# Optimization experiments

Hardware: AMD Instinct MI355X
Metric: run time of the kernel (lower is better)

## Reference

```python
import jax, jax.numpy as jnp
import numpy as np

B, C, H, W = 32, 64, 64, 64
K = 512  # n_embeddings
D = 64   # embedding_dim


def setup_inputs() -> dict:
    key = jax.random.key(0)
    k1, k2 = jax.random.split(key)
    inputs = jax.random.normal(k1, (B, C, H, W), dtype=jnp.float32)
    embedding = jax.random.normal(k2, (K, D), dtype=jnp.float32)
    weight = jnp.ones((K,), dtype=jnp.float32)
    return {"inputs": inputs, "embedding": embedding, "weight": weight}


def reference(inputs, embedding, weight):
    # NCHW -> NHWC, flatten to [N, D]
    x = jnp.transpose(inputs, (0, 2, 3, 1))  # [B,H,W,D]
    input_shape = x.shape
    flat = x.reshape(-1, D)                  # [N,D], N = B*H*W
    n = flat.shape[0]

    usage = jnp.sum(weight >= 0.01)

    # squared Euclidean distances (argmin-equivalent to torch.cdist)
    d2 = (jnp.sum(flat * flat, axis=1, keepdims=True)
          - 2.0 * (flat @ embedding.T)
          + jnp.sum(embedding * embedding, axis=1))  # [N,K]
    indices = jnp.argmin(d2, axis=1)                 # [N]

    # one-hot assignment stats (scatter -> bincount form)
    counts = jnp.zeros((K,), dtype=flat.dtype).at[indices].add(1.0)
    avg_probs = counts / n
    perplexity = jnp.exp(-jnp.sum(avg_probs * jnp.log(avg_probs + 1e-10)))

    # straight-through quantization
    q = embedding[indices].reshape(input_shape)      # [B,H,W,D]
    quantized = jax.lax.stop_gradient(q) + x - jax.lax.stop_gradient(x)

    commitment_loss = jnp.mean((jax.lax.stop_gradient(quantized) - x) ** 2)

    quantized_nchw = jnp.transpose(quantized, (0, 3, 1, 2))
    return quantized_nchw, commitment_loss, perplexity, usage, indices
```

## Files before the change

### kernel.cpp

```cpp
#include <hip/hip_runtime.h>


typedef __attribute__((ext_vector_type(8))) _Float16 f16x8;
typedef __attribute__((ext_vector_type(4))) float f32x4;
typedef unsigned int uint;
typedef unsigned short ushort;

namespace {
constexpr int kC = 64, kH = 64, kW = 64;
constexpr int kK = 512, kD = 64;
constexpr int kHW = kH * kW;
constexpr int kCHW = kC * kHW;
constexpr int kN = 32 * kHW;
constexpr int kQElems = 32 * kC * kHW;
constexpr uint kGapFP = 21u;
}

__device__ __forceinline__ ushort hb(_Float16 h) { return __builtin_bit_cast(ushort, h); }
__device__ __forceinline__ uint umin(uint a, uint b) { return a < b ? a : b; }
__device__ __forceinline__ uint umax(uint a, uint b) { return a > b ? a : b; }

__device__ __forceinline__ void gld16(const void* g, void* l) {
  __builtin_amdgcn_global_load_lds(
      (const __attribute__((address_space(1))) uint*)g,
      (__attribute__((address_space(3))) uint*)l, 16, 0, 0);
}

__global__ __launch_bounds__(64) void vq_prep(const float* __restrict__ emb,
                                              ushort* __restrict__ embPh,
                                              ushort* __restrict__ embPl,
                                              float* __restrict__ embT,
                                              float* __restrict__ enorm,
                                              uint* __restrict__ counts,
                                              uint* __restrict__ flag_count) {
  const int k = blockIdx.x * 64 + threadIdx.x;
  const float4* __restrict__ ep4 = (const float4*)(emb + k * kD);
  float ev[kD];
  uint uh[32], ul[32];
  float s = 0.f;
#pragma unroll
  for (int j = 0; j < kD / 4; ++j) {
    const float4 v = ep4[j];
    ev[4 * j] = v.x; ev[4 * j + 1] = v.y; ev[4 * j + 2] = v.z; ev[4 * j + 3] = v.w;
    s = fmaf(v.x, v.x, s); s = fmaf(v.y, v.y, s);
    s = fmaf(v.z, v.z, s); s = fmaf(v.w, v.w, s);
#pragma unroll
    for (int t = 0; t < 2; ++t) {
      const float e0 = ev[4 * j + 2 * t] * 2048.f;
      const float e1 = ev[4 * j + 2 * t + 1] * 2048.f;
      const _Float16 h0 = (_Float16)e0, h1 = (_Float16)e1;
      const _Float16 l0 = (_Float16)(e0 - (float)h0);
      const _Float16 l1 = (_Float16)(e1 - (float)h1);
      uh[2 * j + t] = (uint)hb(h0) | ((uint)hb(h1) << 16);
      ul[2 * j + t] = (uint)hb(l0) | ((uint)hb(l1) << 16);
    }
  }
  uint4* __restrict__ ph4 = (uint4*)embPh;
  uint4* __restrict__ pl4 = (uint4*)embPl;
#pragma unroll
  for (int cc = 0; cc < 8; ++cc) {
    const int dst = k * 8 + (cc ^ (k & 7));
    ph4[dst] = uint4{uh[4 * cc], uh[4 * cc + 1], uh[4 * cc + 2], uh[4 * cc + 3]};
    pl4[dst] = uint4{ul[4 * cc], ul[4 * cc + 1], ul[4 * cc + 2], ul[4 * cc + 3]};
  }
#pragma unroll
  for (int c = 0; c < kD; ++c) embT[c * kK + k] = ev[c];
  enorm[k] = s;
  counts[k] = 0u;
  if (k == 0) *flag_count = 0u;
}

__global__ __launch_bounds__(512, 4) void vq_assign(
    const float* __restrict__ in, const ushort* __restrict__ embPh,
    const ushort* __restrict__ embPl, const float* __restrict__ embT,
    const float* __restrict__ enorm, float* __restrict__ idx_out,
    float* __restrict__ outq, uint* __restrict__ counts,
    float* __restrict__ partial, uint* __restrict__ flag_count,
    uint* __restrict__ flags, uint flag_cap) {
  __shared__ __align__(16) ushort xbh[128 * 64];
  __shared__ __align__(16) ushort xbl[128 * 64];
  __shared__ __align__(16) ushort ebh[2][4096];
  __shared__ __align__(16) ushort ebl[2][4096];
  __shared__ uint mm1[4][128], mm2[4][128];
  __shared__ float xnp[4][128];
  __shared__ uint hist[512];
  __shared__ uint fidx[128];

  const int tid = threadIdx.x;
  const int lane = tid & 63;
  const int wv = __builtin_amdgcn_readfirstlane(tid >> 6);
  const int ph = wv >> 2;
  const int cs = wv & 3;
  const int c = lane & 15;
  const int g = lane >> 4;

  const int blk = blockIdx.x;
  const int bb = blk >> 5;
  const int hw0 = (blk & 31) << 7;
  const float* __restrict__ xp = in + (size_t)bb * kCHW + hw0 + ph * 64;

  hist[tid] = 0u;

  auto stageE = [&](int buf, int st) {
    const char* gh = (const char*)embPh + st * 8192 + wv * 1024 + lane * 16;
    const char* gl = (const char*)embPl + st * 8192 + wv * 1024 + lane * 16;
    gld16(gh, (char*)&ebh[buf][0] + wv * 1024);
    gld16(gl, (char*)&ebl[buf][0] + wv * 1024);
  };
  stageE(0, 0);

  float en_pre[8];
#pragma unroll
  for (int st = 0; st < 8; ++st)
    en_pre[st] = (enorm[st * 64 + cs * 16 + c] + 256.f) * 2048.f;

  {
    const int p = lane;
    uint uh[8], ul[8];
    float xn = 0.f;
#pragma unroll
    for (int j = 0; j < 8; ++j) {
      const float f0 = xp[(size_t)(cs * 16 + 2 * j) * kHW + p];
      const float f1 = xp[(size_t)(cs * 16 + 2 * j + 1) * kHW + p];
      xn = fmaf(f0, f0, xn);
      xn = fmaf(f1, f1, xn);
      const float m0 = -2.f * f0, m1f = -2.f * f1;
      const _Float16 h0 = (_Float16)m0, h1 = (_Float16)m1f;
      const _Float16 l0 = (_Float16)(m0 - (float)h0);
      const _Float16 l1 = (_Float16)(m1f - (float)h1);
      uh[j] = (uint)hb(h0) | ((uint)hb(h1) << 16);
      ul[j] = (uint)hb(l0) | ((uint)hb(l1) << 16);
    }
    const int row = ph * 64 + p;
    const int swz = (row & 7) << 4;
    const int o0 = (row * 128 + cs * 32) ^ swz;
    const int o1 = (row * 128 + cs * 32 + 16) ^ swz;
    *(uint4*)((char*)xbh + o0) = uint4{uh[0], uh[1], uh[2], uh[3]};
    *(uint4*)((char*)xbh + o1) = uint4{uh[4], uh[5], uh[6], uh[7]};
    *(uint4*)((char*)xbl + o0) = uint4{ul[0], ul[1], ul[2], ul[3]};
    *(uint4*)((char*)xbl + o1) = uint4{ul[4], ul[5], ul[6], ul[7]};
    xnp[cs][row] = xn;
  }
  __syncthreads();

  f16x8 ah[4][2];
  int aoff[4][2];
#pragma unroll
  for (int rt = 0; rt < 4; ++rt)
#pragma unroll
    for (int s = 0; s < 2; ++s) {
      const int row = ph * 64 + rt * 16 + c;
      const int off = (row * 128 + g * 16 + s * 64) ^ ((row & 7) << 4);
      aoff[rt][s] = off;
      ah[rt][s] = *(const f16x8*)((const char*)xbh + off);
    }

  uint m1[16], m2[16];
#pragma unroll
  for (int i = 0; i < 16; ++i) { m1[i] = 0xFFFFFFFFu; m2[i] = 0xFFFFFFFFu; }

#pragma unroll
  for (int st = 0; st < 8; ++st) {
    if (st < 7) stageE((st & 1) ^ 1, st + 1);

    const int rowb = cs * 16 + c;
    const int swb = (rowb & 7) << 4;
    const int ob0 = (rowb * 128 + g * 16) ^ swb;
    const int ob1 = (rowb * 128 + g * 16 + 64) ^ swb;
    const int bsel = st & 1;
    const f16x8 bh0 = *(const f16x8*)((const char*)&ebh[bsel][0] + ob0);
    const f16x8 bh1 = *(const f16x8*)((const char*)&ebh[bsel][0] + ob1);
    const f16x8 bl0 = *(const f16x8*)((const char*)&ebl[bsel][0] + ob0);
    const f16x8 bl1 = *(const f16x8*)((const char*)&ebl[bsel][0] + ob1);
    const float en = en_pre[st];
    const uint kor = (uint)(st * 64 + cs * 16 + c);
    __builtin_amdgcn_s_setprio(1);
#pragma unroll
    for (int rt = 0; rt < 4; ++rt) {
      const f16x8 al0 = *(const f16x8*)((const char*)xbl + aoff[rt][0]);
      const f16x8 al1 = *(const f16x8*)((const char*)xbl + aoff[rt][1]);
      f32x4 acc = {en, en, en, en};
      acc = __builtin_amdgcn_mfma_f32_16x16x32_f16(ah[rt][0], bh0, acc, 0, 0, 0);
      acc = __builtin_amdgcn_mfma_f32_16x16x32_f16(ah[rt][1], bh1, acc, 0, 0, 0);
      acc = __builtin_amdgcn_mfma_f32_16x16x32_f16(ah[rt][0], bl0, acc, 0, 0, 0);
      acc = __builtin_amdgcn_mfma_f32_16x16x32_f16(ah[rt][1], bl1, acc, 0, 0, 0);
      acc = __builtin_amdgcn_mfma_f32_16x16x32_f16(al0, bh0, acc, 0, 0, 0);
      acc = __builtin_amdgcn_mfma_f32_16x16x32_f16(al1, bh1, acc, 0, 0, 0);
#pragma unroll
      for (int r = 0; r < 4; ++r) {
        const uint u = ((uint)acc[r] << 9) | kor;
        const int i = rt * 4 + r;
        const uint t = umax(m1[i], u);
        m1[i] = umin(m1[i], u);
        m2[i] = umin(m2[i], t);
      }
    }
    __builtin_amdgcn_s_setprio(0);
    __syncthreads();
  }

#pragma unroll
  for (int i = 0; i < 16; ++i) {
    uint a1 = m1[i], a2 = m2[i];
#pragma unroll
    for (int off = 1; off < 16; off <<= 1) {
      const uint o1 = __shfl_xor(a1, off, 64);
      const uint o2 = __shfl_xor(a2, off, 64);
      const uint t = umax(a1, o1);
      a1 = umin(a1, o1);
      a2 = umin(umin(a2, o2), t);
    }
    m1[i] = a1; m2[i] = a2;
  }

  if (c == 0) {
#pragma unroll
    for (int i = 0; i < 16; ++i) {
      const int p = ph * 64 + (i >> 2) * 16 + g * 4 + (i & 3);
      mm1[cs][p] = m1[i];
      mm2[cs][p] = m2[i];
    }
  }
  __syncthreads();

  if (tid < 128) {
    uint a1 = mm1[0][tid], a2 = mm2[0][tid];
#pragma unroll
    for (int s = 1; s < 4; ++s) {
      const uint u1 = mm1[s][tid], u2 = mm2[s][tid];
      const uint t = umax(a1, u1);
      a1 = umin(a1, u1);
      a2 = umin(umin(a2, u2), t);
    }
    const uint bidx = a1 & 511u;
    fidx[tid] = bidx;
    idx_out[blk * 128 + tid] = (float)bidx;
    if (((a2 >> 9) - (a1 >> 9)) < kGapFP) {
      const uint slot = atomicAdd(flag_count, 1u);
      if (slot < flag_cap) flags[slot] = (uint)(blk * 128 + tid);
    }
    atomicAdd(&hist[bidx], 1u);

    const float xnorm = (xnp[0][tid] + xnp[1][tid]) + (xnp[2][tid] + xnp[3][tid]);
    float d2 = fmaf((float)(a1 >> 9), 1.f / 2048.f, -256.f) + xnorm;
#pragma unroll
    for (int off = 32; off > 0; off >>= 1) d2 += __shfl_down(d2, off, 64);
    if ((tid & 63) == 0) partial[blk * 2 + (tid >> 6)] = d2;
  }
  __syncthreads();
  if (hist[tid]) atomicAdd(&counts[tid], hist[tid]);

  {
    const int ch = tid >> 3;
    const int wq = tid & 7;
    const float* __restrict__ tr = embT + ch * kK;
    float* __restrict__ oq = outq + (size_t)bb * kCHW + (size_t)ch * kHW + hw0 + wq * 16;
#pragma unroll
    for (int i = 0; i < 4; ++i) {
      const int p0 = wq * 16 + i * 4;
      float4 v;
      v.x = tr[fidx[p0 + 0]];
      v.y = tr[fidx[p0 + 1]];
      v.z = tr[fidx[p0 + 2]];
      v.w = tr[fidx[p0 + 3]];
      *(float4*)(oq + i * 4) = v;
    }
  }
}

__global__ __launch_bounds__(256) void vq_refine(const float* __restrict__ in,
                                                 const float* __restrict__ emb,
                                                 const uint* __restrict__ flag_count,
                                                 const uint* __restrict__ flags,
                                                 uint flag_cap,
                                                 float* __restrict__ idx_out,
                                                 float* __restrict__ outq) {
  uint cnt = *flag_count;
  if (cnt > flag_cap) cnt = flag_cap;
  const int lane = threadIdx.x & 63;
  const uint wave_id = blockIdx.x * 4u + (threadIdx.x >> 6);
  const uint wave_stride = gridDim.x * 4u;

  for (uint i = wave_id; i < cnt; i += wave_stride) {
    const int n = (int)flags[i];
    const int b = n >> 12;
    const int hw = n & 4095;
    const float* __restrict__ xp = in + (size_t)b * kCHW + hw;

    float xr[kD];
#pragma unroll
    for (int d = 0; d < kD; ++d) xr[d] = xp[(size_t)d * kHW];

    double best = 1e300;
    int bidx = 0;
#pragma unroll 1
    for (int kk = 0; kk < 8; ++kk) {
      const int k = lane * 8 + kk;
      const float4* __restrict__ ep4 = (const float4*)(emb + k * kD);
      double s0 = 0.0, s1 = 0.0;
#pragma unroll
      for (int j = 0; j < kD / 4; ++j) {
        const float4 e = ep4[j];
        const double d0 = (double)xr[4 * j + 0] - (double)e.x;
        const double d1 = (double)xr[4 * j + 1] - (double)e.y;
        const double d2 = (double)xr[4 * j + 2] - (double)e.z;
        const double d3 = (double)xr[4 * j + 3] - (double)e.w;
        s0 = fma(d0, d0, s0);
        s1 = fma(d1, d1, s1);
        s0 = fma(d2, d2, s0);
        s1 = fma(d3, d3, s1);
      }
      const double s = s0 + s1;
      if (s < best) { best = s; bidx = k; }
    }
#pragma unroll
    for (int off = 32; off > 0; off >>= 1) {
      const double ob = __shfl_xor(best, off, 64);
      const int oi = __shfl_xor(bidx, off, 64);
      if (ob < best || (ob == best && oi < bidx)) { best = ob; bidx = oi; }
    }
    if (lane == 0) idx_out[n] = (float)bidx;
    outq[(size_t)b * kCHW + (size_t)lane * kHW + hw] = emb[bidx * kD + lane];
  }
}

__global__ __launch_bounds__(512) void vq_finalize(const float* __restrict__ weight,
                                                   const uint* __restrict__ counts,
                                                   const float* __restrict__ partial,
                                                   float* __restrict__ out_scalars) {
  __shared__ float red[512];
  const int t = threadIdx.x;

  const float avg = (float)counts[t] / (float)kN;
  red[t] = avg * logf(avg + 1e-10f);
  __syncthreads();
#pragma unroll
  for (int off = 256; off > 0; off >>= 1) {
    if (t < off) red[t] += red[t + off];
    __syncthreads();
  }
  const float perp = expf(-red[0]);
  __syncthreads();

  red[t] = (partial[t] + partial[t + 512]) + (partial[t + 1024] + partial[t + 1536]);
  __syncthreads();
#pragma unroll
  for (int off = 256; off > 0; off >>= 1) {
    if (t < off) red[t] += red[t + off];
    __syncthreads();
  }
  const float loss = red[0] / (float)((long long)kN * (long long)kD);
  __syncthreads();

  red[t] = (weight[t] >= 0.01f) ? 1.f : 0.f;
  __syncthreads();
#pragma unroll
  for (int off = 256; off > 0; off >>= 1) {
    if (t < off) red[t] += red[t + off];
    __syncthreads();
  }
  if (t == 0) {
    out_scalars[0] = loss;
    out_scalars[1] = perp;
    out_scalars[2] = red[0];
  }
}

extern "C" void kernel_launch(void* const* d_in, const int* in_sizes, int n_in,
                              void* d_out, int out_size, void* d_ws, size_t ws_size,
                              hipStream_t stream) {
  const float* in = (const float*)d_in[0];
  const float* emb = (const float*)d_in[1];
  const float* weight = (const float*)d_in[2];
  float* out = (float*)d_out;

  float* ws_f = (float*)d_ws;
  uint* ws_u = (uint*)d_ws;
  ushort* embPh = (ushort*)d_ws;
  ushort* embPl = embPh + kK * kD;
  float* embT = ws_f + 32768;
  float* enorm = ws_f + 65536;
  uint* counts = ws_u + 66048;
  float* partial = ws_f + 66560;
  uint* flag_count = ws_u + 68608;
  uint* flags = ws_u + 68609;
  const size_t ws_elems = ws_size / 4;
  const uint flag_cap =
      (ws_elems > 68609)
          ? (uint)((ws_elems - 68609 < (size_t)kN) ? ws_elems - 68609 : (size_t)kN)
          : 0u;

  float* outq = out;
  float* out_scalars = out + kQElems;
  float* idx_out = out + kQElems + 3;

  vq_prep<<<8, 64, 0, stream>>>(emb, embPh, embPl, embT, enorm, counts, flag_count);
  vq_assign<<<kN / 128, 512, 0, stream>>>(in, embPh, embPl, embT, enorm, idx_out,
                                          outq, counts, partial, flag_count, flags,
                                          flag_cap);
  vq_refine<<<256, 256, 0, stream>>>(in, emb, flag_count, flags, flag_cap,
                                     idx_out, outq);
  vq_finalize<<<1, 512, 0, stream>>>(weight, counts, partial, out_scalars);
}
```

Baseline: 97.15 us.

## Retile VQ assign into 64-point blocks with a 2x2 wave split

The assign kernel now uses 256-thread blocks covering 64 points instead of 512-thread blocks covering 128 points. Its four waves are arranged as 2 point-groups by 2 code-groups, each handling 32 points by 32 codes per stage. The low-half x fragments are hoisted into registers, and the cross-wave min reduction shrinks from four partners to two. The aim is more, smaller blocks for better scheduling and lower LDS use, at the cost of twice as many embedding stagings from L2 and more B-fragment LDS reads per wave.

```diff
diff --git a/kernel.cpp b/kernel.cpp
--- a/kernel.cpp
+++ b/kernel.cpp
@@ -70,49 +70,55 @@
   if (k == 0) *flag_count = 0u;
 }
 
-__global__ __launch_bounds__(512, 4) void vq_assign(
+__global__ __launch_bounds__(256, 3) void vq_assign(
     const float* __restrict__ in, const ushort* __restrict__ embPh,
     const ushort* __restrict__ embPl, const float* __restrict__ embT,
     const float* __restrict__ enorm, float* __restrict__ idx_out,
     float* __restrict__ outq, uint* __restrict__ counts,
     float* __restrict__ partial, uint* __restrict__ flag_count,
     uint* __restrict__ flags, uint flag_cap) {
-  __shared__ __align__(16) ushort xbh[128 * 64];
-  __shared__ __align__(16) ushort xbl[128 * 64];
+  __shared__ __align__(16) ushort xbh[64 * 64];
+  __shared__ __align__(16) ushort xbl[64 * 64];
   __shared__ __align__(16) ushort ebh[2][4096];
   __shared__ __align__(16) ushort ebl[2][4096];
-  __shared__ uint mm1[4][128], mm2[4][128];
-  __shared__ float xnp[4][128];
+  __shared__ uint mm1[2][64], mm2[2][64];
+  __shared__ float xnp[4][64];
   __shared__ uint hist[512];
-  __shared__ uint fidx[128];
+  __shared__ uint fidx[64];
 
   const int tid = threadIdx.x;
   const int lane = tid & 63;
   const int wv = __builtin_amdgcn_readfirstlane(tid >> 6);
-  const int ph = wv >> 2;
-  const int cs = wv & 3;
+  const int pw = wv >> 1;
+  const int cw = wv & 1;
   const int c = lane & 15;
   const int g = lane >> 4;
 
   const int blk = blockIdx.x;
-  const int bb = blk >> 5;
-  const int hw0 = (blk & 31) << 7;
-  const float* __restrict__ xp = in + (size_t)bb * kCHW + hw0 + ph * 64;
-
-  hist[tid] = 0u;
+  const int bb = blk >> 6;
+  const int hw0 = (blk & 63) << 6;
+  const float* __restrict__ xp = in + (size_t)bb * kCHW + hw0;
+
+  hist[tid] = 0u; hist[tid + 256] = 0u;
 
   auto stageE = [&](int buf, int st) {
-    const char* gh = (const char*)embPh + st * 8192 + wv * 1024 + lane * 16;
-    const char* gl = (const char*)embPl + st * 8192 + wv * 1024 + lane * 16;
-    gld16(gh, (char*)&ebh[buf][0] + wv * 1024);
-    gld16(gl, (char*)&ebl[buf][0] + wv * 1024);
+#pragma unroll
+    for (int i = 0; i < 2; ++i) {
+      const int off = wv * 1024 + i * 4096;
+      gld16((const char*)embPh + (size_t)st * 8192 + off + lane * 16,
+            (char*)&ebh[buf][0] + off);
+      gld16((const char*)embPl + (size_t)st * 8192 + off + lane * 16,
+            (char*)&ebl[buf][0] + off);
+    }
   };
   stageE(0, 0);
 
-  float en_pre[8];
+  float en_pre[16];
 #pragma unroll
   for (int st = 0; st < 8; ++st)
-    en_pre[st] = (enorm[st * 64 + cs * 16 + c] + 256.f) * 2048.f;
+#pragma unroll
+    for (int ct = 0; ct < 2; ++ct)
+      en_pre[st * 2 + ct] = (enorm[st * 64 + cw * 32 + ct * 16 + c] + 256.f) * 2048.f;
 
   {
     const int p = lane;
@@ -120,8 +126,8 @@
     float xn = 0.f;
 #pragma unroll
     for (int j = 0; j < 8; ++j) {
-      const float f0 = xp[(size_t)(cs * 16 + 2 * j) * kHW + p];
-      const float f1 = xp[(size_t)(cs * 16 + 2 * j + 1) * kHW + p];
+      const float f0 = xp[(size_t)(wv * 16 + 2 * j) * kHW + p];
+      const float f1 = xp[(size_t)(wv * 16 + 2 * j + 1) * kHW + p];
       xn = fmaf(f0, f0, xn);
       xn = fmaf(f1, f1, xn);
       const float m0 = -2.f * f0, m1f = -2.f * f1;
@@ -131,28 +137,26 @@
       uh[j] = (uint)hb(h0) | ((uint)hb(h1) << 16);
       ul[j] = (uint)hb(l0) | ((uint)hb(l1) << 16);
     }
-    const int row = ph * 64 + p;
-    const int swz = (row & 7) << 4;
-    const int o0 = (row * 128 + cs * 32) ^ swz;
-    const int o1 = (row * 128 + cs * 32 + 16) ^ swz;
+    const int swz = (p & 7) << 4;
+    const int o0 = (p * 128 + wv * 32) ^ swz;
+    const int o1 = (p * 128 + wv * 32 + 16) ^ swz;
     *(uint4*)((char*)xbh + o0) = uint4{uh[0], uh[1], uh[2], uh[3]};
     *(uint4*)((char*)xbh + o1) = uint4{uh[4], uh[5], uh[6], uh[7]};
     *(uint4*)((char*)xbl + o0) = uint4{ul[0], ul[1], ul[2], ul[3]};
     *(uint4*)((char*)xbl + o1) = uint4{ul[4], ul[5], ul[6], ul[7]};
-    xnp[cs][row] = xn;
-  }
-  __syncthreads();
-
-  f16x8 ah[4][2];
-  int aoff[4][2];
-#pragma unroll
-  for (int rt = 0; rt < 4; ++rt)
+    xnp[wv][p] = xn;
+  }
+  __syncthreads();
+
+  f16x8 ah[2][2], al[2][2];
+#pragma unroll
+  for (int rt = 0; rt < 2; ++rt)
 #pragma unroll
     for (int s = 0; s < 2; ++s) {
-      const int row = ph * 64 + rt * 16 + c;
+      const int row = pw * 32 + rt * 16 + c;
       const int off = (row * 128 + g * 16 + s * 64) ^ ((row & 7) << 4);
-      aoff[rt][s] = off;
       ah[rt][s] = *(const f16x8*)((const char*)xbh + off);
+      al[rt][s] = *(const f16x8*)((const char*)xbl + off);
     }
 
   uint m1[16], m2[16];
@@ -162,40 +166,40 @@
 #pragma unroll
   for (int st = 0; st < 8; ++st) {
     if (st < 7) stageE((st & 1) ^ 1, st + 1);
-
-    const int rowb = cs * 16 + c;
-    const int swb = (rowb & 7) << 4;
-    const int ob0 = (rowb * 128 + g * 16) ^ swb;
-    const int ob1 = (rowb * 128 + g * 16 + 64) ^ swb;
     const int bsel = st & 1;
-    const f16x8 bh0 = *(const f16x8*)((const char*)&ebh[bsel][0] + ob0);
-    const f16x8 bh1 = *(const f16x8*)((const char*)&ebh[bsel][0] + ob1);
-    const f16x8 bl0 = *(const f16x8*)((const char*)&ebl[bsel][0] + ob0);
-    const f16x8 bl1 = *(const f16x8*)((const char*)&ebl[bsel][0] + ob1);
-    const float en = en_pre[st];
-    const uint kor = (uint)(st * 64 + cs * 16 + c);
-    __builtin_amdgcn_s_setprio(1);
-#pragma unroll
-    for (int rt = 0; rt < 4; ++rt) {
-      const f16x8 al0 = *(const f16x8*)((const char*)xbl + aoff[rt][0]);
-      const f16x8 al1 = *(const f16x8*)((const char*)xbl + aoff[rt][1]);
-      f32x4 acc = {en, en, en, en};
-      acc = __builtin_amdgcn_mfma_f32_16x16x32_f16(ah[rt][0], bh0, acc, 0, 0, 0);
-      acc = __builtin_amdgcn_mfma_f32_16x16x32_f16(ah[rt][1], bh1, acc, 0, 0, 0);
-      acc = __builtin_amdgcn_mfma_f32_16x16x32_f16(ah[rt][0], bl0, acc, 0, 0, 0);
-      acc = __builtin_amdgcn_mfma_f32_16x16x32_f16(ah[rt][1], bl1, acc, 0, 0, 0);
-      acc = __builtin_amdgcn_mfma_f32_16x16x32_f16(al0, bh0, acc, 0, 0, 0);
-      acc = __builtin_amdgcn_mfma_f32_16x16x32_f16(al1, bh1, acc, 0, 0, 0);
-#pragma unroll
-      for (int r = 0; r < 4; ++r) {
-        const uint u = ((uint)acc[r] << 9) | kor;
-        const int i = rt * 4 + r;
-        const uint t = umax(m1[i], u);
-        m1[i] = umin(m1[i], u);
-        m2[i] = umin(m2[i], t);
+#pragma unroll
+    for (int ct = 0; ct < 2; ++ct) {
+      const int rowb = cw * 32 + ct * 16 + c;
+      const int swb = (rowb & 7) << 4;
+      const int ob0 = (rowb * 128 + g * 16) ^ swb;
+      const int ob1 = (rowb * 128 + g * 16 + 64) ^ swb;
+      const f16x8 bh0 = *(const f16x8*)((const char*)&ebh[bsel][0] + ob0);
+      const f16x8 bh1 = *(const f16x8*)((const char*)&ebh[bsel][0] + ob1);
+      const f16x8 bl0 = *(const f16x8*)((const char*)&ebl[bsel][0] + ob0);
+      const f16x8 bl1 = *(const f16x8*)((const char*)&ebl[bsel][0] + ob1);
+      const float en = en_pre[st * 2 + ct];
+      const uint kor = (uint)(st * 64 + cw * 32 + ct * 16 + c);
+      __builtin_amdgcn_s_setprio(1);
+#pragma unroll
+      for (int rt = 0; rt < 2; ++rt) {
+        f32x4 acc = {en, en, en, en};
+        acc = __builtin_amdgcn_mfma_f32_16x16x32_f16(ah[rt][0], bh0, acc, 0, 0, 0);
+        acc = __builtin_amdgcn_mfma_f32_16x16x32_f16(ah[rt][1], bh1, acc, 0, 0, 0);
+        acc = __builtin_amdgcn_mfma_f32_16x16x32_f16(ah[rt][0], bl0, acc, 0, 0, 0);
+        acc = __builtin_amdgcn_mfma_f32_16x16x32_f16(ah[rt][1], bl1, acc, 0, 0, 0);
+        acc = __builtin_amdgcn_mfma_f32_16x16x32_f16(al[rt][0], bh0, acc, 0, 0, 0);
+        acc = __builtin_amdgcn_mfma_f32_16x16x32_f16(al[rt][1], bh1, acc, 0, 0, 0);
+#pragma unroll
+        for (int r = 0; r < 4; ++r) {
+          const uint u = ((uint)acc[r] << 9) | kor;
+          const int i = ct * 8 + rt * 4 + r;
+          const uint t = umax(m1[i], u);
+          m1[i] = umin(m1[i], u);
+          m2[i] = umin(m2[i], t);
+        }
       }
-    }
-    __builtin_amdgcn_s_setprio(0);
+      __builtin_amdgcn_s_setprio(0);
+    }
     __syncthreads();
   }
 
@@ -213,31 +217,38 @@
     m1[i] = a1; m2[i] = a2;
   }
 
+#pragma unroll
+  for (int j = 0; j < 8; ++j) {
+    const uint b1 = m1[8 + j], b2 = m2[8 + j];
+    const uint t = umax(m1[j], b1);
+    m1[j] = umin(m1[j], b1);
+    m2[j] = umin(umin(m2[j], b2), t);
+  }
+
   if (c == 0) {
 #pragma unroll
-    for (int i = 0; i < 16; ++i) {
-      const int p = ph * 64 + (i >> 2) * 16 + g * 4 + (i & 3);
-      mm1[cs][p] = m1[i];
-      mm2[cs][p] = m2[i];
-    }
-  }
-  __syncthreads();
-
-  if (tid < 128) {
+    for (int j = 0; j < 8; ++j) {
+      const int p = pw * 32 + (j >> 2) * 16 + g * 4 + (j & 3);
+      mm1[cw][p] = m1[j];
+      mm2[cw][p] = m2[j];
+    }
+  }
+  __syncthreads();
+
+  if (tid < 64) {
     uint a1 = mm1[0][tid], a2 = mm2[0][tid];
-#pragma unroll
-    for (int s = 1; s < 4; ++s) {
-      const uint u1 = mm1[s][tid], u2 = mm2[s][tid];
+    {
+      const uint u1 = mm1[1][tid], u2 = mm2[1][tid];
       const uint t = umax(a1, u1);
       a1 = umin(a1, u1);
       a2 = umin(umin(a2, u2), t);
     }
     const uint bidx = a1 & 511u;
     fidx[tid] = bidx;
-    idx_out[blk * 128 + tid] = (float)bidx;
+    idx_out[blk * 64 + tid] = (float)bidx;
     if (((a2 >> 9) - (a1 >> 9)) < kGapFP) {
       const uint slot = atomicAdd(flag_count, 1u);
-      if (slot < flag_cap) flags[slot] = (uint)(blk * 128 + tid);
+      if (slot < flag_cap) flags[slot] = (uint)(blk * 64 + tid);
     }
     atomicAdd(&hist[bidx], 1u);
 
@@ -245,14 +256,15 @@
     float d2 = fmaf((float)(a1 >> 9), 1.f / 2048.f, -256.f) + xnorm;
 #pragma unroll
     for (int off = 32; off > 0; off >>= 1) d2 += __shfl_down(d2, off, 64);
-    if ((tid & 63) == 0) partial[blk * 2 + (tid >> 6)] = d2;
+    if (tid == 0) partial[blk] = d2;
   }
   __syncthreads();
   if (hist[tid]) atomicAdd(&counts[tid], hist[tid]);
+  if (hist[tid + 256]) atomicAdd(&counts[tid + 256], hist[tid + 256]);
 
   {
-    const int ch = tid >> 3;
-    const int wq = tid & 7;
+    const int ch = tid >> 2;
+    const int wq = tid & 3;
     const float* __restrict__ tr = embT + ch * kK;
     float* __restrict__ oq = outq + (size_t)bb * kCHW + (size_t)ch * kHW + hw0 + wq * 16;
 #pragma unroll
@@ -395,9 +407,9 @@
   float* idx_out = out + kQElems + 3;
 
   vq_prep<<<8, 64, 0, stream>>>(emb, embPh, embPl, embT, enorm, counts, flag_count);
-  vq_assign<<<kN / 128, 512, 0, stream>>>(in, embPh, embPl, embT, enorm, idx_out,
-                                          outq, counts, partial, flag_count, flags,
-                                          flag_cap);
+  vq_assign<<<kN / 64, 256, 0, stream>>>(in, embPh, embPl, embT, enorm, idx_out,
+                                         outq, counts, partial, flag_count, flags,
+                                         flag_cap);
   vq_refine<<<256, 256, 0, stream>>>(in, emb, flag_count, flags, flag_cap,
                                      idx_out, outq);
   vq_finalize<<<1, 512, 0, stream>>>(weight, counts, partial, out_scalars);
```

New measurement: 99.99 us. +2.9%, slower.

## Keep full codebook resident in LDS and loop blocks over four row groups

Applied to the files above, without the earlier changes.

The assign kernel now loads the entire hi/lo fp16 codebook (128 KB) into LDS once per block and runs a persistent-style loop over four 128-row groups, with 256 blocks instead of 1024. This removes the per-block double-buffered codebook restreaming and its stage syncs. The shared histogram is dropped in favour of direct global atomics on counts, and the partial-sum layout changes to one value per group. The huge LDS footprint limits occupancy to one block per CU, and MFMA work can no longer overlap with loads across blocks as before.

```diff
diff --git a/kernel.cpp b/kernel.cpp
--- a/kernel.cpp
+++ b/kernel.cpp
@@ -70,21 +70,23 @@
   if (k == 0) *flag_count = 0u;
 }
 
-__global__ __launch_bounds__(512, 4) void vq_assign(
+__global__ __launch_bounds__(512, 2) void vq_assign(
     const float* __restrict__ in, const ushort* __restrict__ embPh,
     const ushort* __restrict__ embPl, const float* __restrict__ embT,
     const float* __restrict__ enorm, float* __restrict__ idx_out,
     float* __restrict__ outq, uint* __restrict__ counts,
     float* __restrict__ partial, uint* __restrict__ flag_count,
     uint* __restrict__ flags, uint flag_cap) {
-  __shared__ __align__(16) ushort xbh[128 * 64];
-  __shared__ __align__(16) ushort xbl[128 * 64];
-  __shared__ __align__(16) ushort ebh[2][4096];
-  __shared__ __align__(16) ushort ebl[2][4096];
-  __shared__ uint mm1[4][128], mm2[4][128];
-  __shared__ float xnp[4][128];
-  __shared__ uint hist[512];
-  __shared__ uint fidx[128];
+  __shared__ __align__(16) char lds[163840];
+  ushort* __restrict__ Eh = (ushort*)lds;
+  ushort* __restrict__ El = (ushort*)(lds + 65536);
+  char* __restrict__ xbh = lds + 131072;
+  char* __restrict__ xbl = lds + 147456;
+  uint* __restrict__ mm1 = (uint*)(lds + 131072);
+  uint* __restrict__ mm2 = (uint*)(lds + 133120);
+  uint* __restrict__ fidx = (uint*)(lds + 135168);
+  float* __restrict__ xnsum = (float*)(lds + 135680);
+  float* __restrict__ ssum = (float*)(lds + 135712);
 
   const int tid = threadIdx.x;
   const int lane = tid & 63;
@@ -95,176 +97,183 @@
   const int g = lane >> 4;
 
   const int blk = blockIdx.x;
-  const int bb = blk >> 5;
-  const int hw0 = (blk & 31) << 7;
-  const float* __restrict__ xp = in + (size_t)bb * kCHW + hw0 + ph * 64;
-
-  hist[tid] = 0u;
-
-  auto stageE = [&](int buf, int st) {
-    const char* gh = (const char*)embPh + st * 8192 + wv * 1024 + lane * 16;
-    const char* gl = (const char*)embPl + st * 8192 + wv * 1024 + lane * 16;
-    gld16(gh, (char*)&ebh[buf][0] + wv * 1024);
-    gld16(gl, (char*)&ebl[buf][0] + wv * 1024);
-  };
-  stageE(0, 0);
+  const int bb = blk >> 3;
+  const int hwB = (blk & 7) << 9;
+
+#pragma unroll
+  for (int i = 0; i < 8; ++i) {
+    const int off = wv * 1024 + i * 8192;
+    gld16((const char*)embPh + off + lane * 16, (char*)Eh + off);
+    gld16((const char*)embPl + off + lane * 16, (char*)El + off);
+  }
 
   float en_pre[8];
 #pragma unroll
-  for (int st = 0; st < 8; ++st)
-    en_pre[st] = (enorm[st * 64 + cs * 16 + c] + 256.f) * 2048.f;
-
-  {
-    const int p = lane;
-    uint uh[8], ul[8];
+  for (int ct = 0; ct < 8; ++ct)
+    en_pre[ct] = (enorm[cs * 128 + ct * 16 + c] + 256.f) * 2048.f;
+
+#pragma unroll 1
+  for (int grp = 0; grp < 4; ++grp) {
+    const int hw0 = hwB + (grp << 7);
+    const float* __restrict__ xp = in + (size_t)bb * kCHW + hw0 + ph * 64;
+
     float xn = 0.f;
-#pragma unroll
-    for (int j = 0; j < 8; ++j) {
-      const float f0 = xp[(size_t)(cs * 16 + 2 * j) * kHW + p];
-      const float f1 = xp[(size_t)(cs * 16 + 2 * j + 1) * kHW + p];
-      xn = fmaf(f0, f0, xn);
-      xn = fmaf(f1, f1, xn);
-      const float m0 = -2.f * f0, m1f = -2.f * f1;
-      const _Float16 h0 = (_Float16)m0, h1 = (_Float16)m1f;
-      const _Float16 l0 = (_Float16)(m0 - (float)h0);
-      const _Float16 l1 = (_Float16)(m1f - (float)h1);
-      uh[j] = (uint)hb(h0) | ((uint)hb(h1) << 16);
-      ul[j] = (uint)hb(l0) | ((uint)hb(l1) << 16);
-    }
-    const int row = ph * 64 + p;
-    const int swz = (row & 7) << 4;
-    const int o0 = (row * 128 + cs * 32) ^ swz;
-    const int o1 = (row * 128 + cs * 32 + 16) ^ swz;
-    *(uint4*)((char*)xbh + o0) = uint4{uh[0], uh[1], uh[2], uh[3]};
-    *(uint4*)((char*)xbh + o1) = uint4{uh[4], uh[5], uh[6], uh[7]};
-    *(uint4*)((char*)xbl + o0) = uint4{ul[0], ul[1], ul[2], ul[3]};
-    *(uint4*)((char*)xbl + o1) = uint4{ul[4], ul[5], ul[6], ul[7]};
-    xnp[cs][row] = xn;
-  }
-  __syncthreads();
-
-  f16x8 ah[4][2];
-  int aoff[4][2];
-#pragma unroll
-  for (int rt = 0; rt < 4; ++rt)
-#pragma unroll
-    for (int s = 0; s < 2; ++s) {
-      const int row = ph * 64 + rt * 16 + c;
-      const int off = (row * 128 + g * 16 + s * 64) ^ ((row & 7) << 4);
-      aoff[rt][s] = off;
-      ah[rt][s] = *(const f16x8*)((const char*)xbh + off);
-    }
-
-  uint m1[16], m2[16];
-#pragma unroll
-  for (int i = 0; i < 16; ++i) { m1[i] = 0xFFFFFFFFu; m2[i] = 0xFFFFFFFFu; }
-
-#pragma unroll
-  for (int st = 0; st < 8; ++st) {
-    if (st < 7) stageE((st & 1) ^ 1, st + 1);
-
-    const int rowb = cs * 16 + c;
-    const int swb = (rowb & 7) << 4;
-    const int ob0 = (rowb * 128 + g * 16) ^ swb;
-    const int ob1 = (rowb * 128 + g * 16 + 64) ^ swb;
-    const int bsel = st & 1;
-    const f16x8 bh0 = *(const f16x8*)((const char*)&ebh[bsel][0] + ob0);
-    const f16x8 bh1 = *(const f16x8*)((const char*)&ebh[bsel][0] + ob1);
-    const f16x8 bl0 = *(const f16x8*)((const char*)&ebl[bsel][0] + ob0);
-    const f16x8 bl1 = *(const f16x8*)((const char*)&ebl[bsel][0] + ob1);
-    const float en = en_pre[st];
-    const uint kor = (uint)(st * 64 + cs * 16 + c);
-    __builtin_amdgcn_s_setprio(1);
-#pragma unroll
-    for (int rt = 0; rt < 4; ++rt) {
-      const f16x8 al0 = *(const f16x8*)((const char*)xbl + aoff[rt][0]);
-      const f16x8 al1 = *(const f16x8*)((const char*)xbl + aoff[rt][1]);
-      f32x4 acc = {en, en, en, en};
-      acc = __builtin_amdgcn_mfma_f32_16x16x32_f16(ah[rt][0], bh0, acc, 0, 0, 0);
-      acc = __builtin_amdgcn_mfma_f32_16x16x32_f16(ah[rt][1], bh1, acc, 0, 0, 0);
-      acc = __builtin_amdgcn_mfma_f32_16x16x32_f16(ah[rt][0], bl0, acc, 0, 0, 0);
-      acc = __builtin_amdgcn_mfma_f32_16x16x32_f16(ah[rt][1], bl1, acc, 0, 0, 0);
-      acc = __builtin_amdgcn_mfma_f32_16x16x32_f16(al0, bh0, acc, 0, 0, 0);
-      acc = __builtin_amdgcn_mfma_f32_16x16x32_f16(al1, bh1, acc, 0, 0, 0);
-#pragma unroll
-      for (int r = 0; r < 4; ++r) {
-        const uint u = ((uint)acc[r] << 9) | kor;
-        const int i = rt * 4 + r;
-        const uint t = umax(m1[i], u);
-        m1[i] = umin(m1[i], u);
-        m2[i] = umin(m2[i], t);
-      }
-    }
-    __builtin_amdgcn_s_setprio(0);
-    __syncthreads();
-  }
-
-#pragma unroll
-  for (int i = 0; i < 16; ++i) {
-    uint a1 = m1[i], a2 = m2[i];
-#pragma unroll
-    for (int off = 1; off < 16; off <<= 1) {
-      const uint o1 = __shfl_xor(a1, off, 64);
-      const uint o2 = __shfl_xor(a2, off, 64);
-      const uint t = umax(a1, o1);
-      a1 = umin(a1, o1);
-      a2 = umin(umin(a2, o2), t);
-    }
-    m1[i] = a1; m2[i] = a2;
-  }
-
-  if (c == 0) {
+    {
+      const int p = lane;
+      uint uh[8], ul[8];
+#pragma unroll
+      for (int j = 0; j < 8; ++j) {
+        const float f0 = xp[(size_t)(cs * 16 + 2 * j) * kHW + p];
+        const float f1 = xp[(size_t)(cs * 16 + 2 * j + 1) * kHW + p];
+        xn = fmaf(f0, f0, xn);
+        xn = fmaf(f1, f1, xn);
+        const float m0 = -2.f * f0, m1f = -2.f * f1;
+        const _Float16 h0 = (_Float16)m0, h1 = (_Float16)m1f;
+        const _Float16 l0 = (_Float16)(m0 - (float)h0);
+        const _Float16 l1 = (_Float16)(m1f - (float)h1);
+        uh[j] = (uint)hb(h0) | ((uint)hb(h1) << 16);
+        ul[j] = (uint)hb(l0) | ((uint)hb(l1) << 16);
+      }
+      const int row = ph * 64 + p;
+      const int swz = (row & 7) << 4;
+      const int o0 = (row * 128 + cs * 32) ^ swz;
+      const int o1 = (row * 128 + cs * 32 + 16) ^ swz;
+      *(uint4*)(xbh + o0) = uint4{uh[0], uh[1], uh[2], uh[3]};
+      *(uint4*)(xbh + o1) = uint4{uh[4], uh[5], uh[6], uh[7]};
+      *(uint4*)(xbl + o0) = uint4{ul[0], ul[1], ul[2], ul[3]};
+      *(uint4*)(xbl + o1) = uint4{ul[4], ul[5], ul[6], ul[7]};
+    }
+    __syncthreads();
+
+    f16x8 ah[4][2], al[4][2];
+#pragma unroll
+    for (int rt = 0; rt < 4; ++rt)
+#pragma unroll
+      for (int s = 0; s < 2; ++s) {
+        const int row = ph * 64 + rt * 16 + c;
+        const int off = (row * 128 + g * 16 + s * 64) ^ ((row & 7) << 4);
+        ah[rt][s] = *(const f16x8*)(xbh + off);
+        al[rt][s] = *(const f16x8*)(xbl + off);
+      }
+    __syncthreads();
+
+    {
+      float xw = xn;
+#pragma unroll
+      for (int off = 32; off > 0; off >>= 1) xw += __shfl_down(xw, off, 64);
+      if (lane == 0) xnsum[wv] = xw;
+    }
+
+    uint m1[16], m2[16];
+#pragma unroll
+    for (int i = 0; i < 16; ++i) { m1[i] = 0xFFFFFFFFu; m2[i] = 0xFFFFFFFFu; }
+
+#pragma unroll
+    for (int ct = 0; ct < 8; ++ct) {
+      const int k = cs * 128 + ct * 16 + c;
+      const int swb = (k & 7) << 4;
+      const int ob0 = (k * 128 + g * 16) ^ swb;
+      const int ob1 = (k * 128 + g * 16 + 64) ^ swb;
+      const f16x8 bh0 = *(const f16x8*)((const char*)Eh + ob0);
+      const f16x8 bh1 = *(const f16x8*)((const char*)Eh + ob1);
+      const f16x8 bl0 = *(const f16x8*)((const char*)El + ob0);
+      const f16x8 bl1 = *(const f16x8*)((const char*)El + ob1);
+      const float en = en_pre[ct];
+      const uint kor = (uint)k;
+#pragma unroll
+      for (int rt = 0; rt < 4; ++rt) {
+        f32x4 acc = {en, en, en, en};
+        acc = __builtin_amdgcn_mfma_f32_16x16x32_f16(ah[rt][0], bh0, acc, 0, 0, 0);
+        acc = __builtin_amdgcn_mfma_f32_16x16x32_f16(ah[rt][1], bh1, acc, 0, 0, 0);
+        acc = __builtin_amdgcn_mfma_f32_16x16x32_f16(ah[rt][0], bl0, acc, 0, 0, 0);
+        acc = __builtin_amdgcn_mfma_f32_16x16x32_f16(ah[rt][1], bl1, acc, 0, 0, 0);
+        acc = __builtin_amdgcn_mfma_f32_16x16x32_f16(al[rt][0], bh0, acc, 0, 0, 0);
+        acc = __builtin_amdgcn_mfma_f32_16x16x32_f16(al[rt][1], bh1, acc, 0, 0, 0);
+#pragma unroll
+        for (int r = 0; r < 4; ++r) {
+          const uint u = ((uint)acc[r] << 9) | kor;
+          const int i = rt * 4 + r;
+          const uint t = umax(m1[i], u);
+          m1[i] = umin(m1[i], u);
+          m2[i] = umin(m2[i], t);
+        }
+      }
+    }
+
 #pragma unroll
     for (int i = 0; i < 16; ++i) {
-      const int p = ph * 64 + (i >> 2) * 16 + g * 4 + (i & 3);
-      mm1[cs][p] = m1[i];
-      mm2[cs][p] = m2[i];
-    }
-  }
-  __syncthreads();
-
-  if (tid < 128) {
-    uint a1 = mm1[0][tid], a2 = mm2[0][tid];
-#pragma unroll
-    for (int s = 1; s < 4; ++s) {
-      const uint u1 = mm1[s][tid], u2 = mm2[s][tid];
-      const uint t = umax(a1, u1);
-      a1 = umin(a1, u1);
-      a2 = umin(umin(a2, u2), t);
-    }
-    const uint bidx = a1 & 511u;
-    fidx[tid] = bidx;
-    idx_out[blk * 128 + tid] = (float)bidx;
-    if (((a2 >> 9) - (a1 >> 9)) < kGapFP) {
-      const uint slot = atomicAdd(flag_count, 1u);
-      if (slot < flag_cap) flags[slot] = (uint)(blk * 128 + tid);
-    }
-    atomicAdd(&hist[bidx], 1u);
-
-    const float xnorm = (xnp[0][tid] + xnp[1][tid]) + (xnp[2][tid] + xnp[3][tid]);
-    float d2 = fmaf((float)(a1 >> 9), 1.f / 2048.f, -256.f) + xnorm;
-#pragma unroll
-    for (int off = 32; off > 0; off >>= 1) d2 += __shfl_down(d2, off, 64);
-    if ((tid & 63) == 0) partial[blk * 2 + (tid >> 6)] = d2;
-  }
-  __syncthreads();
-  if (hist[tid]) atomicAdd(&counts[tid], hist[tid]);
-
-  {
-    const int ch = tid >> 3;
-    const int wq = tid & 7;
-    const float* __restrict__ tr = embT + ch * kK;
-    float* __restrict__ oq = outq + (size_t)bb * kCHW + (size_t)ch * kHW + hw0 + wq * 16;
-#pragma unroll
-    for (int i = 0; i < 4; ++i) {
-      const int p0 = wq * 16 + i * 4;
-      float4 v;
-      v.x = tr[fidx[p0 + 0]];
-      v.y = tr[fidx[p0 + 1]];
-      v.z = tr[fidx[p0 + 2]];
-      v.w = tr[fidx[p0 + 3]];
-      *(float4*)(oq + i * 4) = v;
-    }
+      uint a1 = m1[i], a2 = m2[i];
+#pragma unroll
+      for (int off = 1; off < 16; off <<= 1) {
+        const uint o1 = __shfl_xor(a1, off, 64);
+        const uint o2 = __shfl_xor(a2, off, 64);
+        const uint t = umax(a1, o1);
+        a1 = umin(a1, o1);
+        a2 = umin(umin(a2, o2), t);
+      }
+      m1[i] = a1; m2[i] = a2;
+    }
+    if (c == 0) {
+#pragma unroll
+      for (int i = 0; i < 16; ++i) {
+        const int p = ph * 64 + (i >> 2) * 16 + g * 4 + (i & 3);
+        mm1[cs * 128 + p] = m1[i];
+        mm2[cs * 128 + p] = m2[i];
+      }
+    }
+    __syncthreads();
+
+    float s0 = 0.f;
+    if (tid < 128) {
+      uint a1 = mm1[tid], a2 = mm2[tid];
+#pragma unroll
+      for (int s = 1; s < 4; ++s) {
+        const uint u1 = mm1[s * 128 + tid], u2 = mm2[s * 128 + tid];
+        const uint t = umax(a1, u1);
+        a1 = umin(a1, u1);
+        a2 = umin(umin(a2, u2), t);
+      }
+      const uint bidx = a1 & 511u;
+      fidx[tid] = bidx;
+      const int n = bb * kHW + hw0 + tid;
+      idx_out[n] = (float)bidx;
+      if (((a2 >> 9) - (a1 >> 9)) < kGapFP) {
+        const uint slot = atomicAdd(flag_count, 1u);
+        if (slot < flag_cap) flags[slot] = (uint)n;
+      }
+      atomicAdd(&counts[bidx], 1u);
+
+      float d2s = fmaf((float)(a1 >> 9), 1.f / 2048.f, -256.f);
+#pragma unroll
+      for (int off = 32; off > 0; off >>= 1) d2s += __shfl_down(d2s, off, 64);
+      if (tid == 64) *ssum = d2s;
+      s0 = d2s;
+    }
+    __syncthreads();
+    if (tid == 0) {
+      float xs = (xnsum[0] + xnsum[1]) + (xnsum[2] + xnsum[3]) +
+                 (xnsum[4] + xnsum[5]) + (xnsum[6] + xnsum[7]);
+      partial[blk * 4 + grp] = s0 + *ssum + xs;
+    }
+
+    {
+      const int ch = tid >> 3;
+      const int wq = tid & 7;
+      const float* __restrict__ tr = embT + ch * kK;
+      float* __restrict__ oq =
+          outq + (size_t)bb * kCHW + (size_t)ch * kHW + hw0 + wq * 16;
+#pragma unroll
+      for (int i = 0; i < 4; ++i) {
+        const int p0 = wq * 16 + i * 4;
+        float4 v;
+        v.x = tr[fidx[p0 + 0]];
+        v.y = tr[fidx[p0 + 1]];
+        v.z = tr[fidx[p0 + 2]];
+        v.w = tr[fidx[p0 + 3]];
+        *(float4*)(oq + i * 4) = v;
+      }
+    }
+    __syncthreads();
   }
 }
 
@@ -342,7 +351,7 @@
   const float perp = expf(-red[0]);
   __syncthreads();
 
-  red[t] = (partial[t] + partial[t + 512]) + (partial[t + 1024] + partial[t + 1536]);
+  red[t] = partial[t] + partial[t + 512];
   __syncthreads();
 #pragma unroll
   for (int off = 256; off > 0; off >>= 1) {
@@ -382,12 +391,12 @@
   float* enorm = ws_f + 65536;
   uint* counts = ws_u + 66048;
   float* partial = ws_f + 66560;
-  uint* flag_count = ws_u + 68608;
-  uint* flags = ws_u + 68609;
+  uint* flag_count = ws_u + 67584;
+  uint* flags = ws_u + 67585;
   const size_t ws_elems = ws_size / 4;
   const uint flag_cap =
-      (ws_elems > 68609)
-          ? (uint)((ws_elems - 68609 < (size_t)kN) ? ws_elems - 68609 : (size_t)kN)
+      (ws_elems > 67585)
+          ? (uint)((ws_elems - 67585 < (size_t)kN) ? ws_elems - 67585 : (size_t)kN)
           : 0u;
 
   float* outq = out;
@@ -395,9 +404,9 @@
   float* idx_out = out + kQElems + 3;
 
   vq_prep<<<8, 64, 0, stream>>>(emb, embPh, embPl, embT, enorm, counts, flag_count);
-  vq_assign<<<kN / 128, 512, 0, stream>>>(in, embPh, embPl, embT, enorm, idx_out,
-                                          outq, counts, partial, flag_count, flags,
-                                          flag_cap);
+  vq_assign<<<256, 512, 0, stream>>>(in, embPh, embPl, embT, enorm, idx_out,
+                                     outq, counts, partial, flag_count, flags,
+                                     flag_cap);
   vq_refine<<<256, 256, 0, stream>>>(in, emb, flag_count, flags, flag_cap,
                                      idx_out, outq);
   vq_finalize<<<1, 512, 0, stream>>>(weight, counts, partial, out_scalars);
```

Result: slower. 128.5 us (+32.2%).
